# Performance work log

Hardware: AMD Instinct MI355X
Metric: run time of the kernel (lower is better)

The kernel has to match this reference:

```python
import jax, jax.numpy as jnp
import numpy as np

COST_CLASS = 2.0
COST_SCREW_MID = 5.0
COST_SCREW_HEAD_TIP = 5.0
GAMMA = 2.0
EPS = 1e-8


def _l1_cdist(a, b):
    # a: [N, d], b: [T, d] -> [N, T] pairwise L1 distance
    return jnp.abs(a[:, None, :] - b[None, :, :]).sum(-1)


def _midpoint(s):
    # screw parameterized as (head_xy, tip_xy); midpoint of the segment
    return (s[:, :2] + s[:, 2:]) * 0.5


def setup_inputs() -> dict:
    key = jax.random.key(0)
    k1, k2, k3, k4 = jax.random.split(key, 4)
    bs, nq, nc = 32, 900, 2
    tpi = 30  # targets per image
    total_tgt = bs * tpi
    return {
        "pred_logits": jax.random.normal(k1, (bs, nq, nc), dtype=jnp.float32),
        "pred_screws": jax.random.uniform(k2, (bs, nq, 4), dtype=jnp.float32),
        "tgt_labels": jax.random.randint(k3, (total_tgt,), 0, nc),
        "tgt_screws": jax.random.uniform(k4, (total_tgt, 4), dtype=jnp.float32),
        "num_targets_per_image": tpi,
    }


def reference(pred_logits, pred_screws, tgt_labels, tgt_screws, num_targets_per_image):
    bs, nq, nc = pred_logits.shape
    out_prob = jax.nn.sigmoid(pred_logits.reshape(bs * nq, nc))  # [N, C]
    out_screws = pred_screws.reshape(bs * nq, 4)                 # [N, 4]

    # focal-style classification cost, gathered at target class ids
    neg_cost = out_prob ** GAMMA * -jnp.log1p(-(out_prob - EPS))  # -log(1 - p + eps)
    pos_cost = (1.0 - out_prob) ** GAMMA * -jnp.log(out_prob + EPS)
    cost_class = pos_cost[:, tgt_labels] - neg_cost[:, tgt_labels]  # [N, T]

    # geometric costs: L1 on midpoint, plus L1 on head and tip endpoints
    cost_mid = _l1_cdist(_midpoint(out_screws), _midpoint(tgt_screws))
    cost_head_tip = (_l1_cdist(out_screws[:, :2], tgt_screws[:, :2])
                     + _l1_cdist(out_screws[:, 2:], tgt_screws[:, 2:]))

    C = (COST_SCREW_MID * cost_mid
         + COST_CLASS * cost_class
         + COST_SCREW_HEAD_TIP * cost_head_tip)
    return C.reshape(bs, nq, -1)  # [bs, num_queries, total_targets]
```

## Files before the change

kernel.cpp:

```cpp
#include <hip/hip_runtime.h>
#include <math.h>


#define NB 16
#define BLOCK 256

typedef float f32x4 __attribute__((ext_vector_type(4)));

__global__ __launch_bounds__(BLOCK) void matcher_kernel(
    const float* __restrict__ logits,
    const float* __restrict__ pscrews,
    const int*   __restrict__ tlabels,
    const float* __restrict__ tscrews,
    float*       __restrict__ out,
    int N, int T)
{
    __shared__ float row[NB][8];
    const int tid = threadIdx.x;
    const int n0  = blockIdx.x * NB;

    if (tid < NB && (n0 + tid) < N) {
        const int n = n0 + tid;
        float4 s = reinterpret_cast<const float4*>(pscrews)[n];
        float hx = s.x, hy = s.y, tx = s.z, ty = s.w;
        row[tid][0] = hx; row[tid][1] = hy;
        row[tid][2] = tx; row[tid][3] = ty;
        row[tid][4] = (hx + tx) * 0.5f;
        row[tid][5] = (hy + ty) * 0.5f;
        float l0 = logits[n * 2 + 0];
        float l1 = logits[n * 2 + 1];
        #pragma unroll
        for (int c = 0; c < 2; ++c) {
            float l = (c == 0) ? l0 : l1;
            float p = 1.0f / (1.0f + expf(-l));
            float om = 1.0f - p;
            float pos = om * om * (-logf(p + 1e-8f));
            float neg = p * p * (-logf(1.0f - p + 1e-8f));
            row[tid][6 + c] = 2.0f * (pos - neg);
        }
    }

    const int chunk = tid;
    const bool active = (chunk * 4 + 3) < T;
    float thx[4], thy[4], ttx[4], tty[4], tmx[4], tmy[4];
    int   lab[4];
    if (active) {
        int4 lb = reinterpret_cast<const int4*>(tlabels)[chunk];
        lab[0] = lb.x; lab[1] = lb.y; lab[2] = lb.z; lab[3] = lb.w;
        #pragma unroll
        for (int j = 0; j < 4; ++j) {
            float4 s = reinterpret_cast<const float4*>(tscrews)[chunk * 4 + j];
            thx[j] = s.x; thy[j] = s.y; ttx[j] = s.z; tty[j] = s.w;
            tmx[j] = (s.x + s.z) * 0.5f;
            tmy[j] = (s.y + s.w) * 0.5f;
        }
    }

    __syncthreads();

    if (!active) return;

    const int tq = T >> 2;
    f32x4* outv = reinterpret_cast<f32x4*>(out) + (size_t)n0 * tq + chunk;

    if (n0 + NB <= N) {
        #pragma unroll
        for (int g = 0; g < NB; g += 4) {
            f32x4 res[4];
            #pragma unroll
            for (int r = 0; r < 4; ++r) {
                const int rr = g + r;
                float4 a = *reinterpret_cast<const float4*>(&row[rr][0]);
                float4 b = *reinterpret_cast<const float4*>(&row[rr][4]);
                float v[4];
                #pragma unroll
                for (int j = 0; j < 4; ++j) {
                    float d = fabsf(a.x - thx[j]) + fabsf(a.y - thy[j])
                            + fabsf(a.z - ttx[j]) + fabsf(a.w - tty[j])
                            + fabsf(b.x - tmx[j]) + fabsf(b.y - tmy[j]);
                    float cc = (lab[j] != 0) ? b.w : b.z;
                    v[j] = fmaf(d, 5.0f, cc);
                }
                res[r].x = v[0]; res[r].y = v[1]; res[r].z = v[2]; res[r].w = v[3];
            }
            #pragma unroll
            for (int r = 0; r < 4; ++r) {
                __builtin_nontemporal_store(res[r], outv + (size_t)(g + r) * tq);
            }
        }
    } else {
        for (int r = 0; r < NB; ++r) {
            const int n = n0 + r;
            if (n >= N) break;
            float4 a = *reinterpret_cast<const float4*>(&row[r][0]);
            float4 b = *reinterpret_cast<const float4*>(&row[r][4]);
            f32x4 res;
            #pragma unroll
            for (int j = 0; j < 4; ++j) {
                float d = fabsf(a.x - thx[j]) + fabsf(a.y - thy[j])
                        + fabsf(a.z - ttx[j]) + fabsf(a.w - tty[j])
                        + fabsf(b.x - tmx[j]) + fabsf(b.y - tmy[j]);
                float cc = (lab[j] != 0) ? b.w : b.z;
                res[j] = fmaf(d, 5.0f, cc);
            }
            __builtin_nontemporal_store(res, outv + (size_t)r * tq);
        }
    }
}

extern "C" void kernel_launch(void* const* d_in, const int* in_sizes, int n_in,
                              void* d_out, int out_size, void* d_ws, size_t ws_size,
                              hipStream_t stream) {
    const float* logits  = (const float*)d_in[0];
    const float* pscrews = (const float*)d_in[1];
    const int*   tlabels = (const int*)d_in[2];
    const float* tscrews = (const float*)d_in[3];
    float* out = (float*)d_out;

    const int N = in_sizes[1] / 4;
    const int T = in_sizes[2];

    const int blocks = (N + NB - 1) / NB;
    matcher_kernel<<<blocks, BLOCK, 0, stream>>>(logits, pscrews, tlabels, tscrews, out, N, T);
}
```

Measured before the change: 129.0 us.

## Split per-row descriptor precompute into separate kernel to drop block sync

Moves the per-prediction row descriptors (coordinates, midpoints, class costs) into a prepass kernel that writes them to workspace. The main matcher kernel then reads them straight from global memory instead of staging them in shared memory behind a __syncthreads. This removes the block barrier and the serialized transcendental work done by 16 threads in every block. The cost is an extra kernel launch and a workspace round trip. A fused fallback is kept for when the workspace is too small.

```diff
diff --git a/kernel.cpp b/kernel.cpp
--- a/kernel.cpp
+++ b/kernel.cpp
@@ -1,47 +1,50 @@
 #include <hip/hip_runtime.h>
 #include <math.h>
+#include <stdint.h>
 
 
+#define BLOCK 256
 #define NB 16
-#define BLOCK 256
 
 typedef float f32x4 __attribute__((ext_vector_type(4)));
 
-__global__ __launch_bounds__(BLOCK) void matcher_kernel(
+__device__ __forceinline__ float class_cost(float l) {
+    float p  = 1.0f / (1.0f + expf(-l));
+    float om = 1.0f - p;
+    float pos = om * om * (-logf(p + 1e-8f));
+    float neg = p * p * (-logf(om + 1e-8f));
+    return 2.0f * (pos - neg);
+}
+
+__global__ __launch_bounds__(BLOCK) void row_desc_kernel(
     const float* __restrict__ logits,
     const float* __restrict__ pscrews,
+    float*       __restrict__ ws,
+    int N)
+{
+    int n = blockIdx.x * BLOCK + threadIdx.x;
+    if (n >= N) return;
+    float4 s = reinterpret_cast<const float4*>(pscrews)[n];
+    float2 l = reinterpret_cast<const float2*>(logits)[n];
+    f32x4 d0 = {s.x, s.y, s.z, s.w};
+    f32x4 d1 = {(s.x + s.z) * 0.5f, (s.y + s.w) * 0.5f, class_cost(l.x), class_cost(l.y)};
+    f32x4* w = reinterpret_cast<f32x4*>(ws) + (size_t)n * 2;
+    w[0] = d0;
+    w[1] = d1;
+}
+
+__global__ __launch_bounds__(BLOCK) void matcher_v3(
+    const float* __restrict__ ws,
     const int*   __restrict__ tlabels,
     const float* __restrict__ tscrews,
     float*       __restrict__ out,
     int N, int T)
 {
-    __shared__ float row[NB][8];
-    const int tid = threadIdx.x;
-    const int n0  = blockIdx.x * NB;
-
-    if (tid < NB && (n0 + tid) < N) {
-        const int n = n0 + tid;
-        float4 s = reinterpret_cast<const float4*>(pscrews)[n];
-        float hx = s.x, hy = s.y, tx = s.z, ty = s.w;
-        row[tid][0] = hx; row[tid][1] = hy;
-        row[tid][2] = tx; row[tid][3] = ty;
-        row[tid][4] = (hx + tx) * 0.5f;
-        row[tid][5] = (hy + ty) * 0.5f;
-        float l0 = logits[n * 2 + 0];
-        float l1 = logits[n * 2 + 1];
-        #pragma unroll
-        for (int c = 0; c < 2; ++c) {
-            float l = (c == 0) ? l0 : l1;
-            float p = 1.0f / (1.0f + expf(-l));
-            float om = 1.0f - p;
-            float pos = om * om * (-logf(p + 1e-8f));
-            float neg = p * p * (-logf(1.0f - p + 1e-8f));
-            row[tid][6 + c] = 2.0f * (pos - neg);
-        }
-    }
-
+    const int tid   = threadIdx.x;
+    const int n0    = blockIdx.x * NB;
     const int chunk = tid;
     const bool active = (chunk * 4 + 3) < T;
+
     float thx[4], thy[4], ttx[4], tty[4], tmx[4], tmy[4];
     int   lab[4];
     if (active) {
@@ -55,13 +58,11 @@
             tmy[j] = (s.y + s.w) * 0.5f;
         }
     }
-
-    __syncthreads();
-
     if (!active) return;
 
     const int tq = T >> 2;
     f32x4* outv = reinterpret_cast<f32x4*>(out) + (size_t)n0 * tq + chunk;
+    const f32x4* w = reinterpret_cast<const f32x4*>(ws) + (size_t)n0 * 2;
 
     if (n0 + NB <= N) {
         #pragma unroll
@@ -69,9 +70,8 @@
             f32x4 res[4];
             #pragma unroll
             for (int r = 0; r < 4; ++r) {
-                const int rr = g + r;
-                float4 a = *reinterpret_cast<const float4*>(&row[rr][0]);
-                float4 b = *reinterpret_cast<const float4*>(&row[rr][4]);
+                f32x4 a = w[(g + r) * 2 + 0];
+                f32x4 b = w[(g + r) * 2 + 1];
                 float v[4];
                 #pragma unroll
                 for (int j = 0; j < 4; ++j) {
@@ -92,8 +92,8 @@
         for (int r = 0; r < NB; ++r) {
             const int n = n0 + r;
             if (n >= N) break;
-            float4 a = *reinterpret_cast<const float4*>(&row[r][0]);
-            float4 b = *reinterpret_cast<const float4*>(&row[r][4]);
+            f32x4 a = w[r * 2 + 0];
+            f32x4 b = w[r * 2 + 1];
             f32x4 res;
             #pragma unroll
             for (int j = 0; j < 4; ++j) {
@@ -105,6 +105,66 @@
             }
             __builtin_nontemporal_store(res, outv + (size_t)r * tq);
         }
+    }
+}
+
+__global__ __launch_bounds__(BLOCK) void matcher_fused(
+    const float* __restrict__ logits,
+    const float* __restrict__ pscrews,
+    const int*   __restrict__ tlabels,
+    const float* __restrict__ tscrews,
+    float*       __restrict__ out,
+    int N, int T)
+{
+    __shared__ float row[NB][8];
+    const int tid = threadIdx.x;
+    const int n0  = blockIdx.x * NB;
+
+    if (tid < NB && (n0 + tid) < N) {
+        const int n = n0 + tid;
+        float4 s = reinterpret_cast<const float4*>(pscrews)[n];
+        row[tid][0] = s.x; row[tid][1] = s.y;
+        row[tid][2] = s.z; row[tid][3] = s.w;
+        row[tid][4] = (s.x + s.z) * 0.5f;
+        row[tid][5] = (s.y + s.w) * 0.5f;
+        row[tid][6] = class_cost(logits[n * 2 + 0]);
+        row[tid][7] = class_cost(logits[n * 2 + 1]);
+    }
+
+    const int chunk = tid;
+    const bool active = (chunk * 4 + 3) < T;
+    float thx[4], thy[4], ttx[4], tty[4], tmx[4], tmy[4];
+    int   lab[4];
+    if (active) {
+        int4 lb = reinterpret_cast<const int4*>(tlabels)[chunk];
+        lab[0] = lb.x; lab[1] = lb.y; lab[2] = lb.z; lab[3] = lb.w;
+        #pragma unroll
+        for (int j = 0; j < 4; ++j) {
+            float4 s = reinterpret_cast<const float4*>(tscrews)[chunk * 4 + j];
+            thx[j] = s.x; thy[j] = s.y; ttx[j] = s.z; tty[j] = s.w;
+            tmx[j] = (s.x + s.z) * 0.5f;
+            tmy[j] = (s.y + s.w) * 0.5f;
+        }
+    }
+    __syncthreads();
+    if (!active) return;
+
+    const int tq = T >> 2;
+    for (int r = 0; r < NB; ++r) {
+        const int n = n0 + r;
+        if (n >= N) break;
+        float4 a = *reinterpret_cast<const float4*>(&row[r][0]);
+        float4 b = *reinterpret_cast<const float4*>(&row[r][4]);
+        f32x4 res;
+        #pragma unroll
+        for (int j = 0; j < 4; ++j) {
+            float d = fabsf(a.x - thx[j]) + fabsf(a.y - thy[j])
+                    + fabsf(a.z - ttx[j]) + fabsf(a.w - tty[j])
+                    + fabsf(b.x - tmx[j]) + fabsf(b.y - tmy[j]);
+            float cc = (lab[j] != 0) ? b.w : b.z;
+            res[j] = fmaf(d, 5.0f, cc);
+        }
+        __builtin_nontemporal_store(res, reinterpret_cast<f32x4*>(out) + (size_t)n * tq + chunk);
     }
 }
 
@@ -120,6 +180,15 @@
     const int N = in_sizes[1] / 4;
     const int T = in_sizes[2];
 
-    const int blocks = (N + NB - 1) / NB;
-    matcher_kernel<<<blocks, BLOCK, 0, stream>>>(logits, pscrews, tlabels, tscrews, out, N, T);
+    const int blocksB = (N + NB - 1) / NB;
+
+    if (ws_size >= (size_t)N * 8 * sizeof(float)) {
+        const int blocksA = (N + BLOCK - 1) / BLOCK;
+        row_desc_kernel<<<blocksA, BLOCK, 0, stream>>>(logits, pscrews, (float*)d_ws, N);
+        matcher_v3<<<blocksB, BLOCK, 0, stream>>>((const float*)d_ws, tlabels, tscrews,
+                                                  out, N, T);
+    } else {
+        matcher_fused<<<blocksB, BLOCK, 0, stream>>>(logits, pscrews, tlabels, tscrews,
+                                                     out, N, T);
+    }
 }
```

Measured after the change: 130.1 us. About the same (+0.8%).
